# Kernel tuning notes

Hardware: AMD Instinct MI355X
Metric: run time of the kernel (lower is better)

The kernel has to match this reference:

```python
import jax, jax.numpy as jnp
import numpy as np
from jax import lax

EPS = 1e-6
NUM_HEADS = 16
BSZ = 4


def _expected_alignment_train(p_choose):
    """p_choose: [B, T, S] -> alpha [B, T, S].
    q_ij = (1-p_{i,j-1}) q_{i,j-1} + a_{i-1,j};  a_ij = p_ij q_ij
    Per-step closed form: a_i = p_i * excl_cumprod(1-p_i) * cumsum(a_{i-1} / excl_cumprod_clamped)
    """
    B, T, S = p_choose.shape
    # safe exclusive cumprod of (1 - p) along src (fairseq exclusive_cumprod with eps clamp)
    one_minus_p = jnp.clip(1.0 - p_choose, EPS, 1.0)
    cp = jnp.cumprod(one_minus_p, axis=2)
    cumprod_1mp = jnp.concatenate([jnp.ones_like(cp[:, :, :1]), cp[:, :, :-1]], axis=2)
    cumprod_1mp_clamp = jnp.clip(cumprod_1mp, EPS, 1.0)

    init_attn = jnp.zeros((B, S), p_choose.dtype).at[:, 0].set(1.0)

    def step(prev_attn, xs):
        p_i, cp_i, cpc_i = xs  # each [B, S]
        alpha_i = jnp.clip(p_i * cp_i * jnp.cumsum(prev_attn / cpc_i, axis=1), 0.0, 1.0)
        return alpha_i, alpha_i

    xs = (jnp.swapaxes(p_choose, 0, 1),
          jnp.swapaxes(cumprod_1mp, 0, 1),
          jnp.swapaxes(cumprod_1mp_clamp, 0, 1))  # [T, B, S]
    _, alpha = lax.scan(step, init_attn, xs)
    alpha = jnp.swapaxes(alpha, 0, 1)  # [B, T, S]

    # mass preservation (no key padding): residual mass onto last source token
    residuals = 1.0 - jnp.clip(jnp.sum(alpha[:, :, :-1], axis=-1), 0.0, 1.0)
    alpha = alpha.at[:, :, -1].set(residuals)
    return alpha


def reference(q_proj, q_proj_dummy=None, *, _unused=None):
    raise NotImplementedError


def reference(q_proj, k_proj, v_proj, out_w, out_b, energy_bias):
    # q_proj/k_proj/v_proj: [bsz*num_heads, len, head_dim]
    energy = jnp.einsum('btd,bsd->bts', q_proj, k_proj) + energy_bias[0]
    p_choose = jax.nn.sigmoid(energy)                       # [B, T, S]
    alpha = _expected_alignment_train(p_choose)
    beta = alpha                                            # hard-aligned: expected_attention = alpha
    attn = jnp.einsum('bts,bsd->btd', beta, v_proj)         # [B, T, head_dim]
    BH, T, D = attn.shape
    attn = jnp.swapaxes(attn, 0, 1).reshape(T, BSZ, NUM_HEADS * D)  # [T, bsz, embed]
    out = attn @ out_w.T + out_b                            # out_proj
    return out, alpha


def setup_inputs():
    key = jax.random.key(0)
    ks = jax.random.split(key, 4)
    BH, T, S, D = 64, 1024, 1024, 64
    E = NUM_HEADS * D
    return {
        'q_proj': jax.random.normal(ks[0], (BH, T, D), jnp.float32) * 0.1,
        'k_proj': jax.random.normal(ks[1], (BH, S, D), jnp.float32) * 0.1,
        'v_proj': jax.random.normal(ks[2], (BH, S, D), jnp.float32),
        'out_w': jax.random.normal(ks[3], (E, E), jnp.float32) * 0.02,
        'out_b': jnp.zeros((E,), jnp.float32),
        'energy_bias': jnp.full((1,), -2.0, jnp.float32),
    }
```

## Files before the change

### kernel.cpp

```cpp
#include <hip/hip_runtime.h>

#define TT 1024
#define SSZ 1024
#define DD 64
#define BHN 64
#define BSZN 4
#define EEN 1024
#define EPSF 1e-6f

using f32x4 = __attribute__((ext_vector_type(4))) float;
using i32x2 = __attribute__((ext_vector_type(2))) int;
using i32x4 = __attribute__((ext_vector_type(4))) int;
using s16x8 = __attribute__((ext_vector_type(8))) short;

__device__ unsigned short g_Pb[(size_t)BHN * TT * SSZ];
__device__ unsigned short g_Vt[(size_t)BHN * DD * SSZ];
__device__ unsigned short g_Wb[(size_t)EEN * EEN];
__device__ unsigned short g_Xb[(size_t)TT * BSZN * EEN];

template<int CTRL, int RM>
__device__ __forceinline__ float f_dpp(float x, float ident) {
  return __builtin_bit_cast(float,
      __builtin_amdgcn_update_dpp(__builtin_bit_cast(int, ident),
                                  __builtin_bit_cast(int, x),
                                  CTRL, RM, 0xF, false));
}

__device__ __forceinline__ float wscan_add(float x) {
  x += f_dpp<0x111, 0xF>(x, 0.0f);
  x += f_dpp<0x112, 0xF>(x, 0.0f);
  x += f_dpp<0x114, 0xF>(x, 0.0f);
  x += f_dpp<0x118, 0xF>(x, 0.0f);
  x += f_dpp<0x142, 0xA>(x, 0.0f);
  x += f_dpp<0x143, 0xC>(x, 0.0f);
  return x;
}

__device__ __forceinline__ float wave_shr1(float x, float ident) {
  return f_dpp<0x138, 0xF>(x, ident);
}

__device__ __forceinline__ f32x4 aload(const float* p) {
  f32x4 r;
  asm volatile("global_load_dwordx4 %0, %1, off" : "=v"(r) : "v"(p));
  return r;
}
__device__ __forceinline__ void astore(float* p, f32x4 v) {
  asm volatile("global_store_dwordx4 %0, %1, off" :: "v"(p), "v"(v) : "memory");
}
__device__ __forceinline__ void astore2(unsigned short* p, i32x2 v) {
  asm volatile("global_store_dwordx2 %0, %1, off" :: "v"(p), "v"(v) : "memory");
}

__device__ __forceinline__ int cvt_pk(float lo, float hi) {
  int r;
  asm("v_cvt_pk_bf16_f32 %0, %1, %2" : "=v"(r) : "v"(lo), "v"(hi));
  return r;
}
__device__ __forceinline__ unsigned short bfr(float x) {
  unsigned u = __builtin_bit_cast(unsigned, x);
  u += 0x7fffu + ((u >> 16) & 1u);
  return (unsigned short)(u >> 16);
}
__device__ __forceinline__ s16x8 pack8p(const float* p) {
  f32x4 a = *(const f32x4*)p;
  f32x4 b = *(const f32x4*)(p + 4);
  i32x4 r;
  r[0] = cvt_pk(a[0], a[1]); r[1] = cvt_pk(a[2], a[3]);
  r[2] = cvt_pk(b[0], b[1]); r[3] = cvt_pk(b[2], b[3]);
  return __builtin_bit_cast(s16x8, r);
}
__device__ __forceinline__ s16x8 pack8f(float v0, float v1, float v2, float v3,
                                        float v4, float v5, float v6, float v7) {
  i32x4 r;
  r[0] = cvt_pk(v0, v1); r[1] = cvt_pk(v2, v3);
  r[2] = cvt_pk(v4, v5); r[3] = cvt_pk(v6, v7);
  return __builtin_bit_cast(s16x8, r);
}

__global__ __launch_bounds__(256) void k_prep_w(const float* __restrict__ W) {
  const size_t idx = ((size_t)blockIdx.x * 256 + threadIdx.x) * 8;
  *(s16x8*)(g_Wb + idx) = pack8p(W + idx);
}

__global__ __launch_bounds__(256) void k_prep_v(const float* __restrict__ V) {
  __shared__ float tile[64][65];
  const int tid = threadIdx.x;
  const int bh = blockIdx.x >> 4;
  const int s0 = (blockIdx.x & 15) << 6;
  {
    const int r = tid >> 2, cq = (tid & 3) << 4;
    const float* src = V + ((size_t)bh * SSZ + s0 + r) * DD + cq;
    *(float4*)&tile[r][cq + 0]  = *(const float4*)(src + 0);
    *(float4*)&tile[r][cq + 4]  = *(const float4*)(src + 4);
    *(float4*)&tile[r][cq + 8]  = *(const float4*)(src + 8);
    *(float4*)&tile[r][cq + 12] = *(const float4*)(src + 12);
  }
  __syncthreads();
  {
    const int d = tid >> 2, sq = (tid & 3) << 4;
    unsigned short* dst = g_Vt + ((size_t)bh * DD + d) * SSZ + s0 + sq;
    *(s16x8*)(dst + 0) = pack8f(tile[sq + 0][d], tile[sq + 1][d], tile[sq + 2][d], tile[sq + 3][d],
                                tile[sq + 4][d], tile[sq + 5][d], tile[sq + 6][d], tile[sq + 7][d]);
    *(s16x8*)(dst + 8) = pack8f(tile[sq + 8][d], tile[sq + 9][d], tile[sq + 10][d], tile[sq + 11][d],
                                tile[sq + 12][d], tile[sq + 13][d], tile[sq + 14][d], tile[sq + 15][d]);
  }
}

__global__ __launch_bounds__(256) void k_energy(const float* __restrict__ Q,
                                                const float* __restrict__ Kp,
                                                const float* __restrict__ eb,
                                                float* __restrict__ P) {
  const int tid = threadIdx.x, w = tid >> 6, l = tid & 63;
  const int rl = l & 15, kg = l >> 4;
  const int bh = blockIdx.x >> 6;
  const int tile = blockIdx.x & 63;
  const int m0 = (tile >> 2) << 6;
  const int n0 = (((tile & 3) << 2) + w) << 6;
  const float* qb = Q + (size_t)bh * TT * DD;
  const float* kb = Kp + (size_t)bh * SSZ * DD;

  f32x4 acc[4][4];
#pragma unroll
  for (int i = 0; i < 4; ++i)
#pragma unroll
    for (int j = 0; j < 4; ++j) acc[i][j] = (f32x4)0.0f;

#pragma unroll
  for (int ks = 0; ks < 2; ++ks) {
    const int kof = (ks << 5) + (kg << 3);
    s16x8 af[4], bf[4];
#pragma unroll
    for (int fi = 0; fi < 4; ++fi)
      af[fi] = pack8p(qb + (size_t)(m0 + fi * 16 + rl) * DD + kof);
#pragma unroll
    for (int fj = 0; fj < 4; ++fj)
      bf[fj] = pack8p(kb + (size_t)(n0 + fj * 16 + rl) * DD + kof);
#pragma unroll
    for (int fi = 0; fi < 4; ++fi)
#pragma unroll
      for (int fj = 0; fj < 4; ++fj)
        acc[fi][fj] = __builtin_amdgcn_mfma_f32_16x16x32_bf16(af[fi], bf[fj], acc[fi][fj], 0, 0, 0);
  }

  const float bias = eb[0];
  float* pb = P + (size_t)bh * TT * SSZ;
#pragma unroll
  for (int fi = 0; fi < 4; ++fi)
#pragma unroll
    for (int r = 0; r < 4; ++r) {
      const size_t rowoff = (size_t)(m0 + fi * 16 + (kg << 2) + r) * SSZ;
#pragma unroll
      for (int fj = 0; fj < 4; ++fj) {
        float x = acc[fi][fj][r] + bias;
        pb[rowoff + n0 + fj * 16 + rl] = __builtin_amdgcn_rcpf(1.0f + __expf(-x));
      }
    }
}

#define STEP(T, QS) do {                                                       \
  const int t_ = (T);                                                          \
  asm volatile("s_waitcnt vmcnt(8)" ::: "memory");                             \
  __builtin_amdgcn_sched_barrier(0);                                           \
  float fn0 = 1.0f - QS.x, fn1 = 1.0f - QS.y, fn2 = 1.0f - QS.z, fn3 = 1.0f - QS.w; \
  { int rr = t_ + 5; if (rr > TT - 1) rr = TT - 1;                             \
    QS = aload(gq + (size_t)rr * SSZ); }                                       \
  float ln0 = fn0, ln1 = ln0 * fn1, ln2 = ln1 * fn2, ln3 = ln2 * fn3;          \
  float An0 = ln3;                                                             \
  float An1 = An0 * f_dpp<0x111, 0xF>(An0, 1.0f);                              \
  float An2 = An1 * f_dpp<0x112, 0xF>(An1, 1.0f);                              \
  float An3 = An2 * f_dpp<0x114, 0xF>(An2, 1.0f);                              \
  float An4 = An3 * f_dpp<0x118, 0xF>(An3, 1.0f);                              \
  float An5 = An4 * f_dpp<0x142, 0xA>(An4, 1.0f);                              \
  float An6 = An5 * f_dpp<0x143, 0xC>(An5, 1.0f);                              \
  float wEn = wave_shr1(An6, 1.0f);                                            \
  float bb0 = fminf(c0  * prev0, prev0);                                       \
  float bb1 = fminf(cl0 * prev1, prev1);                                       \
  float bb2 = fminf(cl1 * prev2, prev2);                                       \
  float bb3 = fminf(cl2 * prev3, prev3);                                       \
  float Blo1 = fmaf(fc0, bb0, bb1);                                            \
  float Blo2 = fmaf(fc1, Blo1, bb2);                                           \
  float Blo3 = fmaf(fc2, Blo2, bb3);                                           \
  float B_ = fc3 * Blo3;                                                       \
  B_ = fmaf(As0, f_dpp<0x111, 0xF>(B_, 0.0f), B_);                             \
  B_ = fmaf(As1, f_dpp<0x112, 0xF>(B_, 0.0f), B_);                             \
  B_ = fmaf(As2, f_dpp<0x114, 0xF>(B_, 0.0f), B_);                             \
  B_ = fmaf(As3, f_dpp<0x118, 0xF>(B_, 0.0f), B_);                             \
  B_ = fmaf(As4, f_dpp<0x142, 0xA>(B_, 0.0f), B_);                             \
  float Bfull = fmaf(As5, f_dpp<0x143, 0xC>(B_, 0.0f), B_);                    \
  float wB = wave_shr1(Bfull, 0.0f);                                           \
  if (lane == 63) ldsAB[t_ & 1][w] = make_float2(An6, Bfull);                  \
  asm volatile("s_waitcnt lgkmcnt(0)" ::: "memory");                           \
  __builtin_amdgcn_s_barrier();                                                \
  __builtin_amdgcn_sched_barrier(0);                                           \
  float2 ab0 = ldsAB[t_ & 1][0];                                               \
  float2 ab1 = ldsAB[t_ & 1][1];                                               \
  float2 ab2 = ldsAB[t_ & 1][2];                                               \
  float Ew = 0.0f;                                                             \
  if (w == 1) Ew = ab0.y;                                                      \
  else if (w == 2) Ew = fmaf(A1g, ab0.y, ab1.y);                               \
  else if (w == 3) Ew = fmaf(A2g, fmaf(A1g, ab0.y, ab1.y), ab2.y);             \
  float El = fmaf(wE, Ew, wB);                                                 \
  float D0 = bb0 + El;                                                         \
  float D1 = fmaf(lc0, El, Blo1);                                              \
  float D2 = fmaf(lc1, El, Blo2);                                              \
  float D3 = fmaf(lc2, El, Blo3);                                              \
  float a0 = fminf(fmaf(-fc0, D0, D0), 1.0f);                                  \
  float a1 = fminf(fmaf(-fc1, D1, D1), 1.0f);                                  \
  float a2 = fminf(fmaf(-fc2, D2, D2), 1.0f);                                  \
  float a3 = fminf(fmaf(-fc3, D3, D3), 1.0f);                                  \
  prev0 = a0; prev1 = a1; prev2 = a2; prev3 = a3;                              \
  f32x4 av4; av4.x = a0; av4.y = a1; av4.z = a2; av4.w = a3;                   \
  if (tid != 255) {                                                            \
    astore(gq + (size_t)t_ * SSZ, av4);                                        \
    i32x2 pk; pk[0] = cvt_pk(a0, a1); pk[1] = cvt_pk(a2, a3);                  \
    astore2(gpb + (size_t)t_ * SSZ, pk);                                       \
  }                                                                            \
  float la = (a0 + a1) + (a2 + a3);                                            \
  float wsum = wscan_add(la);                                                  \
  if (lane == 63 && w < 3) ldsS[t_ & 1][w] = wsum;                             \
  if (tid == 255) {                                                            \
    if (t_ > 0) {                                                              \
      float tot = ldsS[(t_ - 1) & 1][0] + ldsS[(t_ - 1) & 1][1]                \
                + ldsS[(t_ - 1) & 1][2] + wsum_prev;                           \
      float rest = tot - pend.w;                                               \
      pend.w = 1.0f - fminf(fmaxf(rest, 0.0f), 1.0f);                          \
      astore(gq + (size_t)(t_ - 1) * SSZ, pend);                               \
      i32x2 pk2; pk2[0] = cvt_pk(pend.x, pend.y); pk2[1] = cvt_pk(pend.z, pend.w); \
      astore2(gpb + (size_t)(t_ - 1) * SSZ, pk2);                              \
    }                                                                          \
    pend = av4; wsum_prev = wsum;                                              \
  }                                                                            \
  fc0 = fn0; fc1 = fn1; fc2 = fn2; fc3 = fn3;                                  \
  lc0 = ln0; lc1 = ln1; lc2 = ln2;                                             \
  As0 = An0; As1 = An1; As2 = An2; As3 = An3; As4 = An4; As5 = An5;            \
  wE = wEn;                                                                    \
  float Pw_ = 1.0f;                                                            \
  if (w > 0) Pw_ = ab0.x;                                                      \
  if (w > 1) Pw_ *= ab1.x;                                                     \
  if (w > 2) Pw_ *= ab2.x;                                                     \
  c0 = (Pw_ * 1e6f) * wEn;                                                     \
  cl0 = c0 * ln0; cl1 = c0 * ln1; cl2 = c0 * ln2;                              \
  A1g = ab1.x; A2g = ab2.x;                                                    \
} while (0)

__global__ __launch_bounds__(256, 1) void k_scan(float* __restrict__ A) {
  const int b = blockIdx.x;
  const int tid = threadIdx.x;
  const int w = tid >> 6;
  const int lane = tid & 63;
  __shared__ float2 ldsAB[2][4];
  __shared__ float ldsS[2][4];

  float* gq = A + (size_t)b * TT * SSZ + ((size_t)w << 8) + ((size_t)lane << 2);
  unsigned short* gpb = g_Pb + (size_t)b * TT * SSZ + ((size_t)w << 8) + ((size_t)lane << 2);

  f32x4 q0 = aload(gq + (size_t)0 * SSZ);
  f32x4 q1 = aload(gq + (size_t)1 * SSZ);
  f32x4 q2 = aload(gq + (size_t)2 * SSZ);
  f32x4 q3 = aload(gq + (size_t)3 * SSZ);
  asm volatile("s_waitcnt vmcnt(0)" ::: "memory");
  __builtin_amdgcn_sched_barrier(0);

  float fc0 = 1.0f - q0.x, fc1 = 1.0f - q0.y, fc2 = 1.0f - q0.z, fc3 = 1.0f - q0.w;
  q0 = aload(gq + (size_t)4 * SSZ);
  float lc0 = fc0, lc1 = lc0 * fc1, lc2 = lc1 * fc2;
  float lc3 = lc2 * fc3;
  float As0 = lc3;
  float As1 = As0 * f_dpp<0x111, 0xF>(As0, 1.0f);
  float As2 = As1 * f_dpp<0x112, 0xF>(As1, 1.0f);
  float As3 = As2 * f_dpp<0x114, 0xF>(As2, 1.0f);
  float As4 = As3 * f_dpp<0x118, 0xF>(As3, 1.0f);
  float As5 = As4 * f_dpp<0x142, 0xA>(As4, 1.0f);
  float A6  = As5 * f_dpp<0x143, 0xC>(As5, 1.0f);
  float wE = wave_shr1(A6, 1.0f);
  if (lane == 63) ldsAB[1][w] = make_float2(A6, 0.0f);
  asm volatile("s_waitcnt lgkmcnt(0)" ::: "memory");
  __builtin_amdgcn_s_barrier();
  __builtin_amdgcn_sched_barrier(0);
  float2 pab0 = ldsAB[1][0], pab1 = ldsAB[1][1], pab2 = ldsAB[1][2];
  float A1g = pab1.x, A2g = pab2.x;
  float Pw = 1.0f;
  if (w > 0) Pw = pab0.x;
  if (w > 1) Pw *= pab1.x;
  if (w > 2) Pw *= pab2.x;
  float c0 = (Pw * 1e6f) * wE;
  float cl0 = c0 * lc0, cl1 = c0 * lc1, cl2 = c0 * lc2;

  float prev0 = (tid == 0) ? 1.0f : 0.0f;
  float prev1 = 0.0f, prev2 = 0.0f, prev3 = 0.0f;
  f32x4 pend; pend.x = 0.0f; pend.y = 0.0f; pend.z = 0.0f; pend.w = 0.0f;
  float wsum_prev = 0.0f;

  for (int t0 = 0; t0 < TT; t0 += 4) {
    STEP(t0 + 0, q1);
    STEP(t0 + 1, q2);
    STEP(t0 + 2, q3);
    STEP(t0 + 3, q0);
  }

  asm volatile("s_waitcnt lgkmcnt(0)" ::: "memory");
  __builtin_amdgcn_s_barrier();
  __builtin_amdgcn_sched_barrier(0);
  if (tid == 255) {
    float tot = ldsS[(TT - 1) & 1][0] + ldsS[(TT - 1) & 1][1]
              + ldsS[(TT - 1) & 1][2] + wsum_prev;
    float rest = tot - pend.w;
    pend.w = 1.0f - fminf(fmaxf(rest, 0.0f), 1.0f);
    astore(gq + (size_t)(TT - 1) * SSZ, pend);
    i32x2 pk; pk[0] = cvt_pk(pend.x, pend.y); pk[1] = cvt_pk(pend.z, pend.w);
    astore2(gpb + (size_t)(TT - 1) * SSZ, pk);
  }
}

__global__ __launch_bounds__(256) void k_av() {
  const int tid = threadIdx.x, w = tid >> 6, l = tid & 63;
  const int rl = l & 15, kg = l >> 4;
  const int gw = blockIdx.x * 4 + w;
  const int bh = gw >> 6;
  const int t0 = (gw & 63) << 4;

  const unsigned short* ab = g_Pb + ((size_t)bh * TT + t0 + rl) * SSZ;
  const unsigned short* vb = g_Vt + (size_t)bh * DD * SSZ;

  f32x4 acc[4];
#pragma unroll
  for (int j = 0; j < 4; ++j) acc[j] = (f32x4)0.0f;

  for (int kk = 0; kk < 32; ++kk) {
    const int kof = (kk << 5) + (kg << 3);
    s16x8 a = *(const s16x8*)(ab + kof);
#pragma unroll
    for (int fj = 0; fj < 4; ++fj) {
      s16x8 b = *(const s16x8*)(vb + (size_t)(fj * 16 + rl) * SSZ + kof);
      acc[fj] = __builtin_amdgcn_mfma_f32_16x16x32_bf16(a, b, acc[fj], 0, 0, 0);
    }
  }

  const int bz = bh >> 4, hh = bh & 15;
#pragma unroll
  for (int fj = 0; fj < 4; ++fj) {
    const int d = fj * 16 + rl;
#pragma unroll
    for (int r = 0; r < 4; ++r) {
      const int t = t0 + (kg << 2) + r;
      g_Xb[((size_t)t * BSZN + bz) * EEN + hh * DD + d] = bfr(acc[fj][r]);
    }
  }
}

__global__ __launch_bounds__(256) void k_out(const float* __restrict__ Bb,
                                             float* __restrict__ Out) {
  const int tid = threadIdx.x, w = tid >> 6, l = tid & 63;
  const int rl = l & 15, kg = l >> 4;
  const int gw = blockIdx.x * 4 + w;
  const int m0 = (gw >> 4) << 4;
  const int n0 = (gw & 15) << 6;

  const unsigned short* xb = g_Xb + (size_t)(m0 + rl) * EEN;

  f32x4 acc[4];
#pragma unroll
  for (int j = 0; j < 4; ++j) acc[j] = (f32x4)0.0f;

  for (int kk = 0; kk < 32; ++kk) {
    const int kof = (kk << 5) + (kg << 3);
    s16x8 a = *(const s16x8*)(xb + kof);
#pragma unroll
    for (int fj = 0; fj < 4; ++fj) {
      s16x8 b = *(const s16x8*)(g_Wb + (size_t)(n0 + fj * 16 + rl) * EEN + kof);
      acc[fj] = __builtin_amdgcn_mfma_f32_16x16x32_bf16(a, b, acc[fj], 0, 0, 0);
    }
  }

#pragma unroll
  for (int fj = 0; fj < 4; ++fj) {
    const float bias = Bb[n0 + fj * 16 + rl];
#pragma unroll
    for (int r = 0; r < 4; ++r) {
      const int m = m0 + (kg << 2) + r;
      Out[(size_t)m * EEN + n0 + fj * 16 + rl] = acc[fj][r] + bias;
    }
  }
}

extern "C" void kernel_launch(void* const* d_in, const int* in_sizes, int n_in,
                              void* d_out, int out_size, void* d_ws, size_t ws_size,
                              hipStream_t stream) {
  const float* Q  = (const float*)d_in[0];
  const float* K  = (const float*)d_in[1];
  const float* V  = (const float*)d_in[2];
  const float* W  = (const float*)d_in[3];
  const float* Bb = (const float*)d_in[4];
  const float* eb = (const float*)d_in[5];
  float* Out = (float*)d_out;
  float* Alpha = Out + (size_t)TT * BSZN * EEN;

  k_prep_w<<<dim3(512), dim3(256), 0, stream>>>(W);
  k_prep_v<<<dim3(BHN * 16), dim3(256), 0, stream>>>(V);
  k_energy<<<dim3(BHN * 64), dim3(256), 0, stream>>>(Q, K, eb, Alpha);
  k_scan<<<dim3(BHN), dim3(256), 0, stream>>>(Alpha);
  k_av<<<dim3(1024), dim3(256), 0, stream>>>();
  k_out<<<dim3(1024), dim3(256), 0, stream>>>(Bb, Out);
}
```

Baseline: 779.3 us.

## Run alignment scan as single wavefront with 16 elements per lane and LDS prefetch ring

Rewrites k_scan so each batch-head is processed by one 64-lane wavefront, with each lane holding 16 consecutive source positions instead of 4. This removes the per-timestep LDS exchange and s_barrier between four waves, and folds the last-column mass residual into the same wave's scan. Future rows are prefetched into an 8-deep LDS ring with asynchronous global-to-LDS loads. In exchange, each lane runs a longer serial cumprod/cumsum chain per step and uses more registers, with fewer threads in flight per block.

```diff
diff --git a/kernel.cpp b/kernel.cpp
--- a/kernel.cpp
+++ b/kernel.cpp
@@ -9,7 +9,6 @@
 #define EPSF 1e-6f
 
 using f32x4 = __attribute__((ext_vector_type(4))) float;
-using i32x2 = __attribute__((ext_vector_type(2))) int;
 using i32x4 = __attribute__((ext_vector_type(4))) int;
 using s16x8 = __attribute__((ext_vector_type(8))) short;
 
@@ -38,18 +37,6 @@
 
 __device__ __forceinline__ float wave_shr1(float x, float ident) {
   return f_dpp<0x138, 0xF>(x, ident);
-}
-
-__device__ __forceinline__ f32x4 aload(const float* p) {
-  f32x4 r;
-  asm volatile("global_load_dwordx4 %0, %1, off" : "=v"(r) : "v"(p));
-  return r;
-}
-__device__ __forceinline__ void astore(float* p, f32x4 v) {
-  asm volatile("global_store_dwordx4 %0, %1, off" :: "v"(p), "v"(v) : "memory");
-}
-__device__ __forceinline__ void astore2(unsigned short* p, i32x2 v) {
-  asm volatile("global_store_dwordx2 %0, %1, off" :: "v"(p), "v"(v) : "memory");
 }
 
 __device__ __forceinline__ int cvt_pk(float lo, float hi) {
@@ -158,158 +145,135 @@
     }
 }
 
-#define STEP(T, QS) do {                                                       \
-  const int t_ = (T);                                                          \
-  asm volatile("s_waitcnt vmcnt(8)" ::: "memory");                             \
-  __builtin_amdgcn_sched_barrier(0);                                           \
-  float fn0 = 1.0f - QS.x, fn1 = 1.0f - QS.y, fn2 = 1.0f - QS.z, fn3 = 1.0f - QS.w; \
-  { int rr = t_ + 5; if (rr > TT - 1) rr = TT - 1;                             \
-    QS = aload(gq + (size_t)rr * SSZ); }                                       \
-  float ln0 = fn0, ln1 = ln0 * fn1, ln2 = ln1 * fn2, ln3 = ln2 * fn3;          \
-  float An0 = ln3;                                                             \
-  float An1 = An0 * f_dpp<0x111, 0xF>(An0, 1.0f);                              \
-  float An2 = An1 * f_dpp<0x112, 0xF>(An1, 1.0f);                              \
-  float An3 = An2 * f_dpp<0x114, 0xF>(An2, 1.0f);                              \
-  float An4 = An3 * f_dpp<0x118, 0xF>(An3, 1.0f);                              \
-  float An5 = An4 * f_dpp<0x142, 0xA>(An4, 1.0f);                              \
-  float An6 = An5 * f_dpp<0x143, 0xC>(An5, 1.0f);                              \
-  float wEn = wave_shr1(An6, 1.0f);                                            \
-  float bb0 = fminf(c0  * prev0, prev0);                                       \
-  float bb1 = fminf(cl0 * prev1, prev1);                                       \
-  float bb2 = fminf(cl1 * prev2, prev2);                                       \
-  float bb3 = fminf(cl2 * prev3, prev3);                                       \
-  float Blo1 = fmaf(fc0, bb0, bb1);                                            \
-  float Blo2 = fmaf(fc1, Blo1, bb2);                                           \
-  float Blo3 = fmaf(fc2, Blo2, bb3);                                           \
-  float B_ = fc3 * Blo3;                                                       \
-  B_ = fmaf(As0, f_dpp<0x111, 0xF>(B_, 0.0f), B_);                             \
-  B_ = fmaf(As1, f_dpp<0x112, 0xF>(B_, 0.0f), B_);                             \
-  B_ = fmaf(As2, f_dpp<0x114, 0xF>(B_, 0.0f), B_);                             \
-  B_ = fmaf(As3, f_dpp<0x118, 0xF>(B_, 0.0f), B_);                             \
-  B_ = fmaf(As4, f_dpp<0x142, 0xA>(B_, 0.0f), B_);                             \
-  float Bfull = fmaf(As5, f_dpp<0x143, 0xC>(B_, 0.0f), B_);                    \
-  float wB = wave_shr1(Bfull, 0.0f);                                           \
-  if (lane == 63) ldsAB[t_ & 1][w] = make_float2(An6, Bfull);                  \
-  asm volatile("s_waitcnt lgkmcnt(0)" ::: "memory");                           \
-  __builtin_amdgcn_s_barrier();                                                \
-  __builtin_amdgcn_sched_barrier(0);                                           \
-  float2 ab0 = ldsAB[t_ & 1][0];                                               \
-  float2 ab1 = ldsAB[t_ & 1][1];                                               \
-  float2 ab2 = ldsAB[t_ & 1][2];                                               \
-  float Ew = 0.0f;                                                             \
-  if (w == 1) Ew = ab0.y;                                                      \
-  else if (w == 2) Ew = fmaf(A1g, ab0.y, ab1.y);                               \
-  else if (w == 3) Ew = fmaf(A2g, fmaf(A1g, ab0.y, ab1.y), ab2.y);             \
-  float El = fmaf(wE, Ew, wB);                                                 \
-  float D0 = bb0 + El;                                                         \
-  float D1 = fmaf(lc0, El, Blo1);                                              \
-  float D2 = fmaf(lc1, El, Blo2);                                              \
-  float D3 = fmaf(lc2, El, Blo3);                                              \
-  float a0 = fminf(fmaf(-fc0, D0, D0), 1.0f);                                  \
-  float a1 = fminf(fmaf(-fc1, D1, D1), 1.0f);                                  \
-  float a2 = fminf(fmaf(-fc2, D2, D2), 1.0f);                                  \
-  float a3 = fminf(fmaf(-fc3, D3, D3), 1.0f);                                  \
-  prev0 = a0; prev1 = a1; prev2 = a2; prev3 = a3;                              \
-  f32x4 av4; av4.x = a0; av4.y = a1; av4.z = a2; av4.w = a3;                   \
-  if (tid != 255) {                                                            \
-    astore(gq + (size_t)t_ * SSZ, av4);                                        \
-    i32x2 pk; pk[0] = cvt_pk(a0, a1); pk[1] = cvt_pk(a2, a3);                  \
-    astore2(gpb + (size_t)t_ * SSZ, pk);                                       \
-  }                                                                            \
-  float la = (a0 + a1) + (a2 + a3);                                            \
-  float wsum = wscan_add(la);                                                  \
-  if (lane == 63 && w < 3) ldsS[t_ & 1][w] = wsum;                             \
-  if (tid == 255) {                                                            \
-    if (t_ > 0) {                                                              \
-      float tot = ldsS[(t_ - 1) & 1][0] + ldsS[(t_ - 1) & 1][1]                \
-                + ldsS[(t_ - 1) & 1][2] + wsum_prev;                           \
-      float rest = tot - pend.w;                                               \
-      pend.w = 1.0f - fminf(fmaxf(rest, 0.0f), 1.0f);                          \
-      astore(gq + (size_t)(t_ - 1) * SSZ, pend);                               \
-      i32x2 pk2; pk2[0] = cvt_pk(pend.x, pend.y); pk2[1] = cvt_pk(pend.z, pend.w); \
-      astore2(gpb + (size_t)(t_ - 1) * SSZ, pk2);                              \
-    }                                                                          \
-    pend = av4; wsum_prev = wsum;                                              \
-  }                                                                            \
-  fc0 = fn0; fc1 = fn1; fc2 = fn2; fc3 = fn3;                                  \
-  lc0 = ln0; lc1 = ln1; lc2 = ln2;                                             \
-  As0 = An0; As1 = An1; As2 = An2; As3 = An3; As4 = An4; As5 = An5;            \
-  wE = wEn;                                                                    \
-  float Pw_ = 1.0f;                                                            \
-  if (w > 0) Pw_ = ab0.x;                                                      \
-  if (w > 1) Pw_ *= ab1.x;                                                     \
-  if (w > 2) Pw_ *= ab2.x;                                                     \
-  c0 = (Pw_ * 1e6f) * wEn;                                                     \
-  cl0 = c0 * ln0; cl1 = c0 * ln1; cl2 = c0 * ln2;                              \
-  A1g = ab1.x; A2g = ab2.x;                                                    \
-} while (0)
-
-__global__ __launch_bounds__(256, 1) void k_scan(float* __restrict__ A) {
+__global__ __launch_bounds__(64, 1) void k_scan(float* __restrict__ A) {
+  __shared__ float ring[9][1024];
   const int b = blockIdx.x;
-  const int tid = threadIdx.x;
-  const int w = tid >> 6;
-  const int lane = tid & 63;
-  __shared__ float2 ldsAB[2][4];
-  __shared__ float ldsS[2][4];
-
-  float* gq = A + (size_t)b * TT * SSZ + ((size_t)w << 8) + ((size_t)lane << 2);
-  unsigned short* gpb = g_Pb + (size_t)b * TT * SSZ + ((size_t)w << 8) + ((size_t)lane << 2);
-
-  f32x4 q0 = aload(gq + (size_t)0 * SSZ);
-  f32x4 q1 = aload(gq + (size_t)1 * SSZ);
-  f32x4 q2 = aload(gq + (size_t)2 * SSZ);
-  f32x4 q3 = aload(gq + (size_t)3 * SSZ);
+  const int lane = threadIdx.x;
+  float* gq = A + (size_t)b * TT * SSZ + (lane << 4);
+  unsigned short* gpb = g_Pb + (size_t)b * TT * SSZ + (lane << 4);
+
+#pragma unroll
+  for (int r = 0; r < 8; ++r) {
+#pragma unroll
+    for (int j = 0; j < 4; ++j)
+      __builtin_amdgcn_global_load_lds(
+          (const __attribute__((address_space(1))) void*)(gq + (size_t)r * SSZ + j * 4),
+          (__attribute__((address_space(3))) void*)&ring[r][j * 256], 16, 0, 0);
+  }
   asm volatile("s_waitcnt vmcnt(0)" ::: "memory");
   __builtin_amdgcn_sched_barrier(0);
 
-  float fc0 = 1.0f - q0.x, fc1 = 1.0f - q0.y, fc2 = 1.0f - q0.z, fc3 = 1.0f - q0.w;
-  q0 = aload(gq + (size_t)4 * SSZ);
-  float lc0 = fc0, lc1 = lc0 * fc1, lc2 = lc1 * fc2;
-  float lc3 = lc2 * fc3;
-  float As0 = lc3;
-  float As1 = As0 * f_dpp<0x111, 0xF>(As0, 1.0f);
-  float As2 = As1 * f_dpp<0x112, 0xF>(As1, 1.0f);
-  float As3 = As2 * f_dpp<0x114, 0xF>(As2, 1.0f);
-  float As4 = As3 * f_dpp<0x118, 0xF>(As3, 1.0f);
-  float As5 = As4 * f_dpp<0x142, 0xA>(As4, 1.0f);
-  float A6  = As5 * f_dpp<0x143, 0xC>(As5, 1.0f);
-  float wE = wave_shr1(A6, 1.0f);
-  if (lane == 63) ldsAB[1][w] = make_float2(A6, 0.0f);
-  asm volatile("s_waitcnt lgkmcnt(0)" ::: "memory");
-  __builtin_amdgcn_s_barrier();
-  __builtin_amdgcn_sched_barrier(0);
-  float2 pab0 = ldsAB[1][0], pab1 = ldsAB[1][1], pab2 = ldsAB[1][2];
-  float A1g = pab1.x, A2g = pab2.x;
-  float Pw = 1.0f;
-  if (w > 0) Pw = pab0.x;
-  if (w > 1) Pw *= pab1.x;
-  if (w > 2) Pw *= pab2.x;
-  float c0 = (Pw * 1e6f) * wE;
-  float cl0 = c0 * lc0, cl1 = c0 * lc1, cl2 = c0 * lc2;
-
-  float prev0 = (tid == 0) ? 1.0f : 0.0f;
-  float prev1 = 0.0f, prev2 = 0.0f, prev3 = 0.0f;
-  f32x4 pend; pend.x = 0.0f; pend.y = 0.0f; pend.z = 0.0f; pend.w = 0.0f;
-  float wsum_prev = 0.0f;
-
-  for (int t0 = 0; t0 < TT; t0 += 4) {
-    STEP(t0 + 0, q1);
-    STEP(t0 + 1, q2);
-    STEP(t0 + 2, q3);
-    STEP(t0 + 3, q0);
-  }
-
-  asm volatile("s_waitcnt lgkmcnt(0)" ::: "memory");
-  __builtin_amdgcn_s_barrier();
-  __builtin_amdgcn_sched_barrier(0);
-  if (tid == 255) {
-    float tot = ldsS[(TT - 1) & 1][0] + ldsS[(TT - 1) & 1][1]
-              + ldsS[(TT - 1) & 1][2] + wsum_prev;
-    float rest = tot - pend.w;
-    pend.w = 1.0f - fminf(fmaxf(rest, 0.0f), 1.0f);
-    astore(gq + (size_t)(TT - 1) * SSZ, pend);
-    i32x2 pk; pk[0] = cvt_pk(pend.x, pend.y); pk[1] = cvt_pk(pend.z, pend.w);
-    astore2(gpb + (size_t)(TT - 1) * SSZ, pk);
+  f32x4 qc0 = *(f32x4*)&ring[0][0 * 256 + lane * 4];
+  f32x4 qc1 = *(f32x4*)&ring[0][1 * 256 + lane * 4];
+  f32x4 qc2 = *(f32x4*)&ring[0][2 * 256 + lane * 4];
+  f32x4 qc3 = *(f32x4*)&ring[0][3 * 256 + lane * 4];
+
+  float prev[16];
+#pragma unroll
+  for (int i = 0; i < 16; ++i) prev[i] = 0.0f;
+  if (lane == 0) prev[0] = 1.0f;
+
+  for (int t = 0; t < TT; ++t) {
+    asm volatile("s_waitcnt vmcnt(24)" ::: "memory");
+    __builtin_amdgcn_sched_barrier(0);
+    const int sn = (t + 1) & 7;
+    f32x4 qn0 = *(f32x4*)&ring[sn][0 * 256 + lane * 4];
+    f32x4 qn1 = *(f32x4*)&ring[sn][1 * 256 + lane * 4];
+    f32x4 qn2 = *(f32x4*)&ring[sn][2 * 256 + lane * 4];
+    f32x4 qn3 = *(f32x4*)&ring[sn][3 * 256 + lane * 4];
+    {
+      int rr = t + 8;
+      const int sl = (rr <= TT - 1) ? (t & 7) : 8;
+      if (rr > TT - 1) rr = TT - 1;
+#pragma unroll
+      for (int j = 0; j < 4; ++j)
+        __builtin_amdgcn_global_load_lds(
+            (const __attribute__((address_space(1))) void*)(gq + (size_t)rr * SSZ + j * 4),
+            (__attribute__((address_space(3))) void*)&ring[sl][j * 256], 16, 0, 0);
+    }
+
+    float f[16];
+#pragma unroll
+    for (int j = 0; j < 4; ++j) {
+      f[0 + j]  = 1.0f - qc0[j];
+      f[4 + j]  = 1.0f - qc1[j];
+      f[8 + j]  = 1.0f - qc2[j];
+      f[12 + j] = 1.0f - qc3[j];
+    }
+    float l[16];
+    l[0] = f[0];
+#pragma unroll
+    for (int i = 1; i < 16; ++i) l[i] = l[i - 1] * f[i];
+    float fpl = wave_shr1(f[15], 1.0f);
+    float al[8]; al[0] = fpl;
+#pragma unroll
+    for (int i = 1; i < 8; ++i) al[i] = al[i - 1] * f[i - 1];
+    float ah[8]; ah[0] = f[7];
+#pragma unroll
+    for (int j = 1; j < 8; ++j) ah[j] = ah[j - 1] * f[7 + j];
+    float A0 = al[7] * ah[7];
+    float A1 = A0 * f_dpp<0x111, 0xF>(A0, 1.0f);
+    float A2 = A1 * f_dpp<0x112, 0xF>(A1, 1.0f);
+    float A3 = A2 * f_dpp<0x114, 0xF>(A2, 1.0f);
+    float A4 = A3 * f_dpp<0x118, 0xF>(A3, 1.0f);
+    float A5 = A4 * f_dpp<0x142, 0xA>(A4, 1.0f);
+    float A6 = A5 * f_dpp<0x143, 0xC>(A5, 1.0f);
+    float Aexcl = wave_shr1(A6, 1.0f);
+    float wx6 = (Aexcl * fpl) * 1e6f;
+    float bb[16];
+    bb[0] = fminf(wx6 * prev[0], prev[0]);
+#pragma unroll
+    for (int i = 1; i < 16; ++i) bb[i] = fminf((wx6 * l[i - 1]) * prev[i], prev[i]);
+    float Blo[8]; Blo[0] = bb[0];
+#pragma unroll
+    for (int i = 1; i < 8; ++i) Blo[i] = fmaf(f[i - 1], Blo[i - 1], bb[i]);
+    float Bhi[8]; Bhi[0] = bb[8];
+#pragma unroll
+    for (int j = 1; j < 8; ++j) Bhi[j] = fmaf(f[7 + j], Bhi[j - 1], bb[8 + j]);
+    float B_ = fmaf(ah[7], Blo[7], Bhi[7]);
+    B_ = fmaf(A0, f_dpp<0x111, 0xF>(B_, 0.0f), B_);
+    B_ = fmaf(A1, f_dpp<0x112, 0xF>(B_, 0.0f), B_);
+    B_ = fmaf(A2, f_dpp<0x114, 0xF>(B_, 0.0f), B_);
+    B_ = fmaf(A3, f_dpp<0x118, 0xF>(B_, 0.0f), B_);
+    B_ = fmaf(A4, f_dpp<0x142, 0xA>(B_, 0.0f), B_);
+    B_ = fmaf(A5, f_dpp<0x143, 0xC>(B_, 0.0f), B_);
+    float carry = wave_shr1(B_, 0.0f);
+    float D[16];
+#pragma unroll
+    for (int i = 0; i < 8; ++i) D[i] = fmaf(al[i], carry, Blo[i]);
+#pragma unroll
+    for (int j = 0; j < 8; ++j) D[8 + j] = fmaf(ah[j], D[7], Bhi[j]);
+    float a[16];
+#pragma unroll
+    for (int i = 0; i < 16; ++i) {
+      a[i] = fminf(fmaf(-f[i], D[i], D[i]), 1.0f);
+      prev[i] = a[i];
+    }
+    float s0_ = (a[0] + a[1]) + (a[2] + a[3]);
+    float s1_ = (a[4] + a[5]) + (a[6] + a[7]);
+    float s2_ = (a[8] + a[9]) + (a[10] + a[11]);
+    float s3_ = (a[12] + a[13]) + (a[14] + a[15]);
+    float tot = wscan_add((s0_ + s1_) + (s2_ + s3_));
+    if (lane == 63)
+      a[15] = 1.0f - fminf(fmaxf(tot - a[15], 0.0f), 1.0f);
+    {
+      float* sb = gq + (size_t)t * SSZ;
+      f32x4 v0 = {a[0], a[1], a[2], a[3]};
+      f32x4 v1 = {a[4], a[5], a[6], a[7]};
+      f32x4 v2 = {a[8], a[9], a[10], a[11]};
+      f32x4 v3 = {a[12], a[13], a[14], a[15]};
+      *(f32x4*)(sb + 0) = v0;  *(f32x4*)(sb + 4) = v1;
+      *(f32x4*)(sb + 8) = v2;  *(f32x4*)(sb + 12) = v3;
+      unsigned short* pbp = gpb + (size_t)t * SSZ;
+      i32x4 pk0, pk1;
+      pk0[0] = cvt_pk(a[0], a[1]);   pk0[1] = cvt_pk(a[2], a[3]);
+      pk0[2] = cvt_pk(a[4], a[5]);   pk0[3] = cvt_pk(a[6], a[7]);
+      pk1[0] = cvt_pk(a[8], a[9]);   pk1[1] = cvt_pk(a[10], a[11]);
+      pk1[2] = cvt_pk(a[12], a[13]); pk1[3] = cvt_pk(a[14], a[15]);
+      *(i32x4*)(pbp + 0) = pk0;
+      *(i32x4*)(pbp + 8) = pk1;
+    }
+    qc0 = qn0; qc1 = qn1; qc2 = qn2; qc3 = qn3;
   }
 }
 
@@ -399,7 +363,7 @@
   k_prep_w<<<dim3(512), dim3(256), 0, stream>>>(W);
   k_prep_v<<<dim3(BHN * 16), dim3(256), 0, stream>>>(V);
   k_energy<<<dim3(BHN * 64), dim3(256), 0, stream>>>(Q, K, eb, Alpha);
-  k_scan<<<dim3(BHN), dim3(256), 0, stream>>>(Alpha);
+  k_scan<<<dim3(BHN), dim3(64), 0, stream>>>(Alpha);
   k_av<<<dim3(1024), dim3(256), 0, stream>>>();
   k_out<<<dim3(1024), dim3(256), 0, stream>>>(Bb, Out);
 }
```

Measured after the change: 916.4 us. 1.18x slower.
